# Kernel tuning notes

Measured on AMD Instinct MI355X. Metric: run time of the kernel, lower is better.

The kernel has to match this reference:

```python
import jax, jax.numpy as jnp
import numpy as np

N = 100000
F = 128

def shifted_softplus(x):
    return jax.nn.softplus(x) - jnp.log(2.0).astype(x.dtype)

def setup_inputs() -> dict:
    key = jax.random.key(0)
    ks = jax.random.split(key, 8)
    scale = 1.0 / np.sqrt(F)
    s = jax.random.normal(ks[0], (N, F), dtype=jnp.float32)
    v = jax.random.normal(ks[1], (N, F, 3), dtype=jnp.float32)
    U_w = jax.random.uniform(ks[2], (F, F), dtype=jnp.float32, minval=-scale, maxval=scale)
    V_w = jax.random.uniform(ks[3], (F, F), dtype=jnp.float32, minval=-scale, maxval=scale)
    scale2 = 1.0 / np.sqrt(2 * F)
    a_w1 = jax.random.uniform(ks[4], (F, 2 * F), dtype=jnp.float32, minval=-scale2, maxval=scale2)
    a_b1 = jax.random.uniform(ks[5], (F,), dtype=jnp.float32, minval=-scale2, maxval=scale2)
    a_w2 = jax.random.uniform(ks[6], (3 * F, F), dtype=jnp.float32, minval=-scale, maxval=scale)
    a_b2 = jax.random.uniform(ks[7], (3 * F,), dtype=jnp.float32, minval=-scale, maxval=scale)
    return {"s": s, "v": v, "U_w": U_w, "V_w": V_w,
            "a_w1": a_w1, "a_b1": a_b1, "a_w2": a_w2, "a_b2": a_b2}

def reference(s, v, U_w, V_w, a_w1, a_b1, a_w2, a_b2):
    # Vector linears along feature dim: (N,F,3) x (Fout,Fin) -> (N,F,3)
    Uv = jnp.einsum('nfc,gf->ngc', v, U_w)
    Vv = jnp.einsum('nfc,gf->ngc', v, V_w)
    Vv_norm_sq = jnp.sum(Vv * Vv, axis=-1)          # (N,F)
    mlp_in = jnp.concatenate([s, Vv_norm_sq], axis=-1)  # (N,2F)
    h = shifted_softplus(mlp_in @ a_w1.T + a_b1)     # (N,F)
    a = h @ a_w2.T + a_b2                            # (N,3F)
    a_ss, a_sv, a_vv = jnp.split(a, 3, axis=-1)
    inner = jnp.sum(Uv * Vv, axis=-1)                # (N,F)
    s_new = s + a_ss + a_sv * inner
    v_new = v + a_vv[:, :, None] * Uv
    return (s_new, v_new)
```

## Files before the change

### kernel.cpp

```cpp
#include <hip/hip_runtime.h>

#define F 128
#define TILE 32
#define NTHR 512
#define NBLK 256

typedef __attribute__((ext_vector_type(8))) __bf16 bf16x8;
typedef __attribute__((ext_vector_type(4))) float f32x4;
typedef __attribute__((ext_vector_type(8))) unsigned short us8;
typedef __attribute__((ext_vector_type(4))) unsigned short us4;
typedef __attribute__((ext_vector_type(2))) unsigned short us2;

struct f3 { float x, y, z; };

__device__ __forceinline__ unsigned short f2bf(float x) {
    __bf16 h = (__bf16)x;
    return __builtin_bit_cast(unsigned short, h);
}
__device__ __forceinline__ float bf2f(unsigned short u) {
    unsigned x = ((unsigned)u) << 16;
    return __builtin_bit_cast(float, x);
}
__device__ __forceinline__ bf16x8 pack8(float4 a, float4 b) {
    us8 t;
    t[0] = f2bf(a.x); t[1] = f2bf(a.y); t[2] = f2bf(a.z); t[3] = f2bf(a.w);
    t[4] = f2bf(b.x); t[5] = f2bf(b.y); t[6] = f2bf(b.z); t[7] = f2bf(b.w);
    return __builtin_bit_cast(bf16x8, t);
}

__device__ __forceinline__ void gload16(const float* g, const unsigned short* l) {
    __builtin_amdgcn_global_load_lds(
        (const __attribute__((address_space(1))) void*)g,
        (__attribute__((address_space(3))) void*)l, 16, 0, 0);
}

#define RAWV 0
#define A1B  24576
#define A1S  136
#define A2B  37632
#define A2S  264
#define A3B  46080
#define A3S  136
#define SHSZ 50432

__global__ __launch_bounds__(256)
void prep_w(const float* __restrict__ Uw, const float* __restrict__ Vw,
            const float* __restrict__ aw1, const float* __restrict__ aw2,
            unsigned short* __restrict__ wbf)
{
    int i = (blockIdx.x * 256 + threadIdx.x) * 4;
    const float* src; int off;
    if (i < 16384)      { src = Uw;  off = i; }
    else if (i < 32768) { src = Vw;  off = i - 16384; }
    else if (i < 65536) { src = aw1; off = i - 32768; }
    else                { src = aw2; off = i - 65536; }
    float4 x = *(const float4*)&src[off];
    us4 o;
    o[0] = f2bf(x.x); o[1] = f2bf(x.y); o[2] = f2bf(x.z); o[3] = f2bf(x.w);
    *(us4*)&wbf[i] = o;
}

template<bool PRE>
__global__ __launch_bounds__(NTHR) __attribute__((amdgpu_waves_per_eu(2, 2)))
void painn_main(const float* __restrict__ s, const float* __restrict__ v,
                const float* __restrict__ Uw, const float* __restrict__ Vw,
                const float* __restrict__ aw1, const float* __restrict__ ab1,
                const float* __restrict__ aw2, const float* __restrict__ ab2,
                const unsigned short* __restrict__ wbf,
                float* __restrict__ out, int Ntot)
{
    __shared__ __align__(16) unsigned short SH[SHSZ];

    const int tid  = threadIdx.x;
    const int lane = tid & 63;
    const int w    = tid >> 6;
    const int l15  = lane & 15;
    const int kp   = lane >> 4;
    const int col  = (w << 4) | l15;
    const size_t NF = (size_t)Ntot * F;
    const int NT   = Ntot / TILE;

    const unsigned short* wU  = wbf;
    const unsigned short* wV  = wbf + 16384;
    const unsigned short* wW1 = wbf + 32768;
    const unsigned short* wW2 = wbf + 65536;

    const float b1  = ab1[col];
    const float bss = ab2[col];
    const float bsv = ab2[F + col];
    const float bvv = ab2[2 * F + col];

    const int vf0  = lane << 1;
    const int srow = tid >> 4;
    const int sf0  = (tid & 15) << 3;

    const float* rawv = (const float*)&SH[RAWV];

    float4 sp0, sp1;

    {
        int t0 = blockIdx.x;
        const float* vsrc = v + (size_t)t0 * TILE * 384;
        #pragma unroll
        for (int j = 0; j < 6; ++j) {
            int ofs = (w + j * 8) * 256;
            gload16(vsrc + ofs + lane * 4, &SH[RAWV + ofs * 2]);
        }
        const float* ssrc = s + (size_t)t0 * TILE * 128 + srow * 128 + sf0;
        sp0 = *(const float4*)ssrc;
        sp1 = *(const float4*)(ssrc + 4);
    }
    asm volatile("s_waitcnt vmcnt(0)" ::: "memory");

    for (int t = blockIdx.x; t < NT; t += NBLK) {
        asm volatile("s_waitcnt vmcnt(8)" ::: "memory");
        __builtin_amdgcn_s_barrier();

        bf16x8 bU[4], bV[4], bW1[8], bWs[4], bWt[4], bWv[4];
        if constexpr (PRE) {
            #pragma unroll
            for (int ks = 0; ks < 4; ++ks) {
                int k0 = (ks << 5) + (kp << 3);
                bU[ks]  = *(const bf16x8*)&wU[col * F + k0];
                bV[ks]  = *(const bf16x8*)&wV[col * F + k0];
                bWs[ks] = *(const bf16x8*)&wW2[(0 * F + col) * F + k0];
                bWt[ks] = *(const bf16x8*)&wW2[(1 * F + col) * F + k0];
                bWv[ks] = *(const bf16x8*)&wW2[(2 * F + col) * F + k0];
            }
            #pragma unroll
            for (int ks = 0; ks < 8; ++ks) {
                int k0 = (ks << 5) + (kp << 3);
                bW1[ks] = *(const bf16x8*)&wW1[col * 256 + k0];
            }
        } else {
            #pragma unroll
            for (int ks = 0; ks < 4; ++ks) {
                int k0 = (ks << 5) + (kp << 3);
                const float4* p;
                p = (const float4*)&Uw[col * F + k0];              bU[ks]  = pack8(p[0], p[1]);
                p = (const float4*)&Vw[col * F + k0];              bV[ks]  = pack8(p[0], p[1]);
                p = (const float4*)&aw2[(size_t)(0*F+col)*F + k0]; bWs[ks] = pack8(p[0], p[1]);
                p = (const float4*)&aw2[(size_t)(1*F+col)*F + k0]; bWt[ks] = pack8(p[0], p[1]);
                p = (const float4*)&aw2[(size_t)(2*F+col)*F + k0]; bWv[ks] = pack8(p[0], p[1]);
            }
            #pragma unroll
            for (int ks = 0; ks < 8; ++ks) {
                int k0 = (ks << 5) + (kp << 3);
                const float4* p = (const float4*)&aw1[col * 256 + k0];
                bW1[ks] = pack8(p[0], p[1]);
            }
        }
        __builtin_amdgcn_sched_barrier(0);

        #pragma unroll
        for (int it = 0; it < 4; ++it) {
            int nl = w + (it << 3);
            const float2* src = (const float2*)&rawv[nl * 384 + vf0 * 3];
            float2 ab = src[0], cd = src[1], ef = src[2];
            us2 p;
            p[0] = f2bf(ab.x); p[1] = f2bf(cd.y); *(us2*)&SH[A1B + (0 * TILE + nl) * A1S + vf0] = p;
            p[0] = f2bf(ab.y); p[1] = f2bf(ef.x); *(us2*)&SH[A1B + (1 * TILE + nl) * A1S + vf0] = p;
            p[0] = f2bf(cd.x); p[1] = f2bf(ef.y); *(us2*)&SH[A1B + (2 * TILE + nl) * A1S + vf0] = p;
        }
        {
            us4 t0, t1;
            t0[0] = f2bf(sp0.x); t0[1] = f2bf(sp0.y); t0[2] = f2bf(sp0.z); t0[3] = f2bf(sp0.w);
            t1[0] = f2bf(sp1.x); t1[1] = f2bf(sp1.y); t1[2] = f2bf(sp1.z); t1[3] = f2bf(sp1.w);
            *(us4*)&SH[A2B + srow * A2S + sf0]     = t0;
            *(us4*)&SH[A2B + srow * A2S + sf0 + 4] = t1;
        }
        asm volatile("s_waitcnt lgkmcnt(0)" ::: "memory");
        __builtin_amdgcn_s_barrier();
        __builtin_amdgcn_sched_barrier(0);

        if (t + NBLK < NT) {
            int t2 = t + NBLK;
            const float* vsrc = v + (size_t)t2 * TILE * 384;
            #pragma unroll
            for (int j = 0; j < 6; ++j) {
                int ofs = (w + j * 8) * 256;
                gload16(vsrc + ofs + lane * 4, &SH[RAWV + ofs * 2]);
            }
            const float* ssrc = s + (size_t)t2 * TILE * 128 + srow * 128 + sf0;
            sp0 = *(const float4*)ssrc;
            sp1 = *(const float4*)(ssrc + 4);
        }
        __builtin_amdgcn_sched_barrier(0);

        float inr[2][4], nrm[2][4];
        us4 pU[6];
        #pragma unroll
        for (int nt = 0; nt < 2; ++nt)
            #pragma unroll
            for (int r = 0; r < 4; ++r) { inr[nt][r] = 0.f; nrm[nt][r] = 0.f; }
        #pragma unroll
        for (int c = 0; c < 3; ++c) {
            f32x4 aU[2], aV[2];
            aU[0] = (f32x4){0.f,0.f,0.f,0.f}; aU[1] = (f32x4){0.f,0.f,0.f,0.f};
            aV[0] = (f32x4){0.f,0.f,0.f,0.f}; aV[1] = (f32x4){0.f,0.f,0.f,0.f};
            #pragma unroll
            for (int ks = 0; ks < 4; ++ks) {
                #pragma unroll
                for (int nt = 0; nt < 2; ++nt) {
                    bf16x8 a = *(const bf16x8*)&SH[A1B + ((c * 2 + nt) * 16 + l15) * A1S + (ks << 5) + (kp << 3)];
                    aU[nt] = __builtin_amdgcn_mfma_f32_16x16x32_bf16(a, bU[ks], aU[nt], 0, 0, 0);
                    aV[nt] = __builtin_amdgcn_mfma_f32_16x16x32_bf16(a, bV[ks], aV[nt], 0, 0, 0);
                }
            }
            #pragma unroll
            for (int nt = 0; nt < 2; ++nt) {
                us4 q;
                #pragma unroll
                for (int r = 0; r < 4; ++r) {
                    nrm[nt][r] += aV[nt][r] * aV[nt][r];
                    inr[nt][r] += aU[nt][r] * aV[nt][r];
                    q[r] = f2bf(aU[nt][r]);
                }
                pU[c * 2 + nt] = q;
            }
        }
        #pragma unroll
        for (int nt = 0; nt < 2; ++nt) {
            #pragma unroll
            for (int r = 0; r < 4; ++r) {
                int row = nt * 16 + (kp << 2) + r;
                SH[A2B + row * A2S + 128 + col] = f2bf(nrm[nt][r]);
            }
        }
        asm volatile("s_waitcnt lgkmcnt(0)" ::: "memory");
        __builtin_amdgcn_s_barrier();

        f32x4 accH[2];
        accH[0] = (f32x4){0.f,0.f,0.f,0.f}; accH[1] = (f32x4){0.f,0.f,0.f,0.f};
        #pragma unroll
        for (int ks = 0; ks < 8; ++ks) {
            int k0 = (ks << 5) + (kp << 3);
            #pragma unroll
            for (int nt = 0; nt < 2; ++nt) {
                bf16x8 a = *(const bf16x8*)&SH[A2B + (nt * 16 + l15) * A2S + k0];
                accH[nt] = __builtin_amdgcn_mfma_f32_16x16x32_bf16(a, bW1[ks], accH[nt], 0, 0, 0);
            }
        }
        #pragma unroll
        for (int nt = 0; nt < 2; ++nt) {
            #pragma unroll
            for (int r = 0; r < 4; ++r) {
                float x = accH[nt][r] + b1;
                float hsp = fmaxf(x, 0.f) + __logf(1.f + __expf(-fabsf(x))) - 0.69314718056f;
                int row = nt * 16 + (kp << 2) + r;
                SH[A3B + row * A3S + col] = f2bf(hsp);
            }
        }
        asm volatile("s_waitcnt lgkmcnt(0)" ::: "memory");
        __builtin_amdgcn_s_barrier();

        f32x4 accA[2], accS[2], accT[2];
        #pragma unroll
        for (int i = 0; i < 2; ++i) {
            accA[i] = (f32x4){0.f,0.f,0.f,0.f};
            accS[i] = (f32x4){0.f,0.f,0.f,0.f};
            accT[i] = (f32x4){0.f,0.f,0.f,0.f};
        }
        #pragma unroll
        for (int ks = 0; ks < 4; ++ks) {
            int k0 = (ks << 5) + (kp << 3);
            #pragma unroll
            for (int nt = 0; nt < 2; ++nt) {
                bf16x8 a = *(const bf16x8*)&SH[A3B + (nt * 16 + l15) * A3S + k0];
                accS[nt] = __builtin_amdgcn_mfma_f32_16x16x32_bf16(a, bWs[ks], accS[nt], 0, 0, 0);
                accT[nt] = __builtin_amdgcn_mfma_f32_16x16x32_bf16(a, bWt[ks], accT[nt], 0, 0, 0);
                accA[nt] = __builtin_amdgcn_mfma_f32_16x16x32_bf16(a, bWv[ks], accA[nt], 0, 0, 0);
            }
        }

        #pragma unroll
        for (int nt = 0; nt < 2; ++nt) {
            #pragma unroll
            for (int r = 0; r < 4; ++r) {
                int nl = nt * 16 + (kp << 2) + r;
                int n  = t * TILE + nl;
                float avv = accA[nt][r] + bvv;
                size_t base = ((size_t)n * F + col) * 3;
                f3 val;
                val.x = bf2f(SH[A1B + (0 * TILE + nl) * A1S + col]) + avv * bf2f(pU[0 * 2 + nt][r]);
                val.y = bf2f(SH[A1B + (1 * TILE + nl) * A1S + col]) + avv * bf2f(pU[1 * 2 + nt][r]);
                val.z = bf2f(SH[A1B + (2 * TILE + nl) * A1S + col]) + avv * bf2f(pU[2 * 2 + nt][r]);
                *(f3*)&out[NF + base] = val;
                float sres = bf2f(SH[A2B + nl * A2S + col]);
                out[(size_t)n * F + col] = sres + (accS[nt][r] + bss) + (accT[nt][r] + bsv) * inr[nt][r];
            }
        }
    }
}

extern "C" void kernel_launch(void* const* d_in, const int* in_sizes, int n_in,
                              void* d_out, int out_size, void* d_ws, size_t ws_size,
                              hipStream_t stream) {
    (void)n_in; (void)out_size;
    const float* s   = (const float*)d_in[0];
    const float* v   = (const float*)d_in[1];
    const float* Uw  = (const float*)d_in[2];
    const float* Vw  = (const float*)d_in[3];
    const float* aw1 = (const float*)d_in[4];
    const float* ab1 = (const float*)d_in[5];
    const float* aw2 = (const float*)d_in[6];
    const float* ab2 = (const float*)d_in[7];
    float* out = (float*)d_out;
    int Ntot = in_sizes[0] / F;

    if (ws_size >= 114688u * sizeof(unsigned short)) {
        unsigned short* wbf = (unsigned short*)d_ws;
        hipLaunchKernelGGL(prep_w, dim3(112), dim3(256), 0, stream, Uw, Vw, aw1, aw2, wbf);
        hipLaunchKernelGGL((painn_main<true>), dim3(NBLK), dim3(NTHR), 0, stream,
                           s, v, Uw, Vw, aw1, ab1, aw2, ab2, wbf, out, Ntot);
    } else {
        hipLaunchKernelGGL((painn_main<false>), dim3(NBLK), dim3(NTHR), 0, stream,
                           s, v, Uw, Vw, aw1, ab1, aw2, ab2, (const unsigned short*)nullptr, out, Ntot);
    }
}
```

Measured before the change: 187.2 us.

## Replace persistent pipelined kernel with one-tile-per-block non-persistent grid

Drops the persistent 256-block loop with software prefetch of the next tile. Instead it launches one 256-thread block per 16-row tile (6250 blocks), and each wave now computes two 16-column groups. Weights are reloaded from global/L2 per block for the W1/W2 stages rather than kept in registers across tiles, and LDS use is halved so more blocks can be resident per CU. The aim is to rely on occupancy and hardware scheduling to hide latency, at the cost of repeated weight loads and losing the explicit load/compute overlap.

Result: slower. 212.7 us (+13.6%).

```diff
diff --git a/kernel.cpp b/kernel.cpp
--- a/kernel.cpp
+++ b/kernel.cpp
@@ -1,9 +1,8 @@
 #include <hip/hip_runtime.h>
 
 #define F 128
-#define TILE 32
-#define NTHR 512
-#define NBLK 256
+#define TILE 16
+#define NTHR 256
 
 typedef __attribute__((ext_vector_type(8))) __bf16 bf16x8;
 typedef __attribute__((ext_vector_type(4))) float f32x4;
@@ -35,13 +34,13 @@
 }
 
 #define RAWV 0
-#define A1B  24576
+#define A1B  12288
 #define A1S  136
-#define A2B  37632
+#define A2B  18816
 #define A2S  264
-#define A3B  46080
+#define A3B  23040
 #define A3S  136
-#define SHSZ 50432
+#define SHSZ 25216
 
 __global__ __launch_bounds__(256)
 void prep_w(const float* __restrict__ Uw, const float* __restrict__ Vw,
@@ -61,7 +60,7 @@
 }
 
 template<bool PRE>
-__global__ __launch_bounds__(NTHR) __attribute__((amdgpu_waves_per_eu(2, 2)))
+__global__ __launch_bounds__(NTHR) __attribute__((amdgpu_waves_per_eu(3)))
 void painn_main(const float* __restrict__ s, const float* __restrict__ v,
                 const float* __restrict__ Uw, const float* __restrict__ Vw,
                 const float* __restrict__ aw1, const float* __restrict__ ab1,
@@ -76,20 +75,16 @@
     const int w    = tid >> 6;
     const int l15  = lane & 15;
     const int kp   = lane >> 4;
-    const int col  = (w << 4) | l15;
+    const int colA = (w << 4) | l15;
+    const int colB = 64 + ((w << 4) | l15);
     const size_t NF = (size_t)Ntot * F;
-    const int NT   = Ntot / TILE;
+    const int t    = blockIdx.x;
 
     const unsigned short* wU  = wbf;
     const unsigned short* wV  = wbf + 16384;
     const unsigned short* wW1 = wbf + 32768;
     const unsigned short* wW2 = wbf + 65536;
 
-    const float b1  = ab1[col];
-    const float bss = ab2[col];
-    const float bsv = ab2[F + col];
-    const float bvv = ab2[2 * F + col];
-
     const int vf0  = lane << 1;
     const int srow = tid >> 4;
     const int sf0  = (tid & 15) << 3;
@@ -97,198 +92,187 @@
     const float* rawv = (const float*)&SH[RAWV];
 
     float4 sp0, sp1;
-
     {
-        int t0 = blockIdx.x;
-        const float* vsrc = v + (size_t)t0 * TILE * 384;
-        #pragma unroll
-        for (int j = 0; j < 6; ++j) {
-            int ofs = (w + j * 8) * 256;
-            gload16(vsrc + ofs + lane * 4, &SH[RAWV + ofs * 2]);
-        }
-        const float* ssrc = s + (size_t)t0 * TILE * 128 + srow * 128 + sf0;
+        const float* ssrc = s + (size_t)t * TILE * 128 + srow * 128 + sf0;
         sp0 = *(const float4*)ssrc;
         sp1 = *(const float4*)(ssrc + 4);
     }
+    bf16x8 bU[2][4], bV[2][4];
+    #pragma unroll
+    for (int g = 0; g < 2; ++g) {
+        int colg = g ? colB : colA;
+        #pragma unroll
+        for (int ks = 0; ks < 4; ++ks) {
+            int k0 = (ks << 5) + (kp << 3);
+            if constexpr (PRE) {
+                bU[g][ks] = *(const bf16x8*)&wU[colg * F + k0];
+                bV[g][ks] = *(const bf16x8*)&wV[colg * F + k0];
+            } else {
+                const float4* pu = (const float4*)&Uw[colg * F + k0];
+                bU[g][ks] = pack8(pu[0], pu[1]);
+                const float4* pv = (const float4*)&Vw[colg * F + k0];
+                bV[g][ks] = pack8(pv[0], pv[1]);
+            }
+        }
+    }
+    {
+        const float* vsrc = v + (size_t)t * TILE * 384;
+        #pragma unroll
+        for (int j = 0; j < 6; ++j) {
+            int ofs = (w + j * 4) * 256;
+            gload16(vsrc + ofs + lane * 4, &SH[RAWV + ofs * 2]);
+        }
+    }
     asm volatile("s_waitcnt vmcnt(0)" ::: "memory");
-
-    for (int t = blockIdx.x; t < NT; t += NBLK) {
-        asm volatile("s_waitcnt vmcnt(8)" ::: "memory");
-        __builtin_amdgcn_s_barrier();
-
-        bf16x8 bU[4], bV[4], bW1[8], bWs[4], bWt[4], bWv[4];
-        if constexpr (PRE) {
+    __builtin_amdgcn_s_barrier();
+
+    #pragma unroll
+    for (int it = 0; it < 4; ++it) {
+        int idx = tid + it * 256;
+        int nl  = idx >> 6;
+        int f0  = (idx & 63) << 1;
+        const float2* src = (const float2*)&rawv[nl * 384 + f0 * 3];
+        float2 ab = src[0], cd = src[1], ef = src[2];
+        us2 p;
+        p[0] = f2bf(ab.x); p[1] = f2bf(cd.y); *(us2*)&SH[A1B + (0 * TILE + nl) * A1S + f0] = p;
+        p[0] = f2bf(ab.y); p[1] = f2bf(ef.x); *(us2*)&SH[A1B + (1 * TILE + nl) * A1S + f0] = p;
+        p[0] = f2bf(cd.x); p[1] = f2bf(ef.y); *(us2*)&SH[A1B + (2 * TILE + nl) * A1S + f0] = p;
+    }
+    {
+        us4 t0, t1;
+        t0[0] = f2bf(sp0.x); t0[1] = f2bf(sp0.y); t0[2] = f2bf(sp0.z); t0[3] = f2bf(sp0.w);
+        t1[0] = f2bf(sp1.x); t1[1] = f2bf(sp1.y); t1[2] = f2bf(sp1.z); t1[3] = f2bf(sp1.w);
+        *(us4*)&SH[A2B + srow * A2S + sf0]     = t0;
+        *(us4*)&SH[A2B + srow * A2S + sf0 + 4] = t1;
+    }
+    asm volatile("s_waitcnt lgkmcnt(0)" ::: "memory");
+    __builtin_amdgcn_s_barrier();
+
+    float nrm[2][4], inr[2][4];
+    us4 pU[2][3];
+    #pragma unroll
+    for (int c = 0; c < 3; ++c) {
+        f32x4 aU[2], aV[2];
+        aU[0] = (f32x4){0.f,0.f,0.f,0.f}; aU[1] = (f32x4){0.f,0.f,0.f,0.f};
+        aV[0] = (f32x4){0.f,0.f,0.f,0.f}; aV[1] = (f32x4){0.f,0.f,0.f,0.f};
+        #pragma unroll
+        for (int ks = 0; ks < 4; ++ks) {
+            bf16x8 a = *(const bf16x8*)&SH[A1B + (c * TILE + l15) * A1S + (ks << 5) + (kp << 3)];
             #pragma unroll
-            for (int ks = 0; ks < 4; ++ks) {
-                int k0 = (ks << 5) + (kp << 3);
-                bU[ks]  = *(const bf16x8*)&wU[col * F + k0];
-                bV[ks]  = *(const bf16x8*)&wV[col * F + k0];
-                bWs[ks] = *(const bf16x8*)&wW2[(0 * F + col) * F + k0];
-                bWt[ks] = *(const bf16x8*)&wW2[(1 * F + col) * F + k0];
-                bWv[ks] = *(const bf16x8*)&wW2[(2 * F + col) * F + k0];
-            }
-            #pragma unroll
-            for (int ks = 0; ks < 8; ++ks) {
-                int k0 = (ks << 5) + (kp << 3);
-                bW1[ks] = *(const bf16x8*)&wW1[col * 256 + k0];
-            }
-        } else {
-            #pragma unroll
-            for (int ks = 0; ks < 4; ++ks) {
-                int k0 = (ks << 5) + (kp << 3);
-                const float4* p;
-                p = (const float4*)&Uw[col * F + k0];              bU[ks]  = pack8(p[0], p[1]);
-                p = (const float4*)&Vw[col * F + k0];              bV[ks]  = pack8(p[0], p[1]);
-                p = (const float4*)&aw2[(size_t)(0*F+col)*F + k0]; bWs[ks] = pack8(p[0], p[1]);
-                p = (const float4*)&aw2[(size_t)(1*F+col)*F + k0]; bWt[ks] = pack8(p[0], p[1]);
-                p = (const float4*)&aw2[(size_t)(2*F+col)*F + k0]; bWv[ks] = pack8(p[0], p[1]);
-            }
-            #pragma unroll
-            for (int ks = 0; ks < 8; ++ks) {
-                int k0 = (ks << 5) + (kp << 3);
-                const float4* p = (const float4*)&aw1[col * 256 + k0];
-                bW1[ks] = pack8(p[0], p[1]);
-            }
-        }
-        __builtin_amdgcn_sched_barrier(0);
-
-        #pragma unroll
-        for (int it = 0; it < 4; ++it) {
-            int nl = w + (it << 3);
-            const float2* src = (const float2*)&rawv[nl * 384 + vf0 * 3];
-            float2 ab = src[0], cd = src[1], ef = src[2];
-            us2 p;
-            p[0] = f2bf(ab.x); p[1] = f2bf(cd.y); *(us2*)&SH[A1B + (0 * TILE + nl) * A1S + vf0] = p;
-            p[0] = f2bf(ab.y); p[1] = f2bf(ef.x); *(us2*)&SH[A1B + (1 * TILE + nl) * A1S + vf0] = p;
-            p[0] = f2bf(cd.x); p[1] = f2bf(ef.y); *(us2*)&SH[A1B + (2 * TILE + nl) * A1S + vf0] = p;
-        }
-        {
-            us4 t0, t1;
-            t0[0] = f2bf(sp0.x); t0[1] = f2bf(sp0.y); t0[2] = f2bf(sp0.z); t0[3] = f2bf(sp0.w);
-            t1[0] = f2bf(sp1.x); t1[1] = f2bf(sp1.y); t1[2] = f2bf(sp1.z); t1[3] = f2bf(sp1.w);
-            *(us4*)&SH[A2B + srow * A2S + sf0]     = t0;
-            *(us4*)&SH[A2B + srow * A2S + sf0 + 4] = t1;
-        }
-        asm volatile("s_waitcnt lgkmcnt(0)" ::: "memory");
-        __builtin_amdgcn_s_barrier();
-        __builtin_amdgcn_sched_barrier(0);
-
-        if (t + NBLK < NT) {
-            int t2 = t + NBLK;
-            const float* vsrc = v + (size_t)t2 * TILE * 384;
-            #pragma unroll
-            for (int j = 0; j < 6; ++j) {
-                int ofs = (w + j * 8) * 256;
-                gload16(vsrc + ofs + lane * 4, &SH[RAWV + ofs * 2]);
-            }
-            const float* ssrc = s + (size_t)t2 * TILE * 128 + srow * 128 + sf0;
-            sp0 = *(const float4*)ssrc;
-            sp1 = *(const float4*)(ssrc + 4);
-        }
-        __builtin_amdgcn_sched_barrier(0);
-
-        float inr[2][4], nrm[2][4];
-        us4 pU[6];
-        #pragma unroll
-        for (int nt = 0; nt < 2; ++nt)
-            #pragma unroll
-            for (int r = 0; r < 4; ++r) { inr[nt][r] = 0.f; nrm[nt][r] = 0.f; }
-        #pragma unroll
-        for (int c = 0; c < 3; ++c) {
-            f32x4 aU[2], aV[2];
-            aU[0] = (f32x4){0.f,0.f,0.f,0.f}; aU[1] = (f32x4){0.f,0.f,0.f,0.f};
-            aV[0] = (f32x4){0.f,0.f,0.f,0.f}; aV[1] = (f32x4){0.f,0.f,0.f,0.f};
-            #pragma unroll
-            for (int ks = 0; ks < 4; ++ks) {
-                #pragma unroll
-                for (int nt = 0; nt < 2; ++nt) {
-                    bf16x8 a = *(const bf16x8*)&SH[A1B + ((c * 2 + nt) * 16 + l15) * A1S + (ks << 5) + (kp << 3)];
-                    aU[nt] = __builtin_amdgcn_mfma_f32_16x16x32_bf16(a, bU[ks], aU[nt], 0, 0, 0);
-                    aV[nt] = __builtin_amdgcn_mfma_f32_16x16x32_bf16(a, bV[ks], aV[nt], 0, 0, 0);
-                }
-            }
-            #pragma unroll
-            for (int nt = 0; nt < 2; ++nt) {
-                us4 q;
-                #pragma unroll
-                for (int r = 0; r < 4; ++r) {
-                    nrm[nt][r] += aV[nt][r] * aV[nt][r];
-                    inr[nt][r] += aU[nt][r] * aV[nt][r];
-                    q[r] = f2bf(aU[nt][r]);
-                }
-                pU[c * 2 + nt] = q;
-            }
-        }
-        #pragma unroll
-        for (int nt = 0; nt < 2; ++nt) {
+            for (int g = 0; g < 2; ++g) {
+                aU[g] = __builtin_amdgcn_mfma_f32_16x16x32_bf16(a, bU[g][ks], aU[g], 0, 0, 0);
+                aV[g] = __builtin_amdgcn_mfma_f32_16x16x32_bf16(a, bV[g][ks], aV[g], 0, 0, 0);
+            }
+        }
+        #pragma unroll
+        for (int g = 0; g < 2; ++g) {
+            us4 q;
             #pragma unroll
             for (int r = 0; r < 4; ++r) {
-                int row = nt * 16 + (kp << 2) + r;
-                SH[A2B + row * A2S + 128 + col] = f2bf(nrm[nt][r]);
-            }
-        }
-        asm volatile("s_waitcnt lgkmcnt(0)" ::: "memory");
-        __builtin_amdgcn_s_barrier();
-
-        f32x4 accH[2];
-        accH[0] = (f32x4){0.f,0.f,0.f,0.f}; accH[1] = (f32x4){0.f,0.f,0.f,0.f};
-        #pragma unroll
-        for (int ks = 0; ks < 8; ++ks) {
-            int k0 = (ks << 5) + (kp << 3);
-            #pragma unroll
-            for (int nt = 0; nt < 2; ++nt) {
-                bf16x8 a = *(const bf16x8*)&SH[A2B + (nt * 16 + l15) * A2S + k0];
-                accH[nt] = __builtin_amdgcn_mfma_f32_16x16x32_bf16(a, bW1[ks], accH[nt], 0, 0, 0);
-            }
-        }
-        #pragma unroll
-        for (int nt = 0; nt < 2; ++nt) {
-            #pragma unroll
-            for (int r = 0; r < 4; ++r) {
-                float x = accH[nt][r] + b1;
-                float hsp = fmaxf(x, 0.f) + __logf(1.f + __expf(-fabsf(x))) - 0.69314718056f;
-                int row = nt * 16 + (kp << 2) + r;
-                SH[A3B + row * A3S + col] = f2bf(hsp);
-            }
-        }
-        asm volatile("s_waitcnt lgkmcnt(0)" ::: "memory");
-        __builtin_amdgcn_s_barrier();
-
-        f32x4 accA[2], accS[2], accT[2];
-        #pragma unroll
-        for (int i = 0; i < 2; ++i) {
-            accA[i] = (f32x4){0.f,0.f,0.f,0.f};
-            accS[i] = (f32x4){0.f,0.f,0.f,0.f};
-            accT[i] = (f32x4){0.f,0.f,0.f,0.f};
-        }
-        #pragma unroll
-        for (int ks = 0; ks < 4; ++ks) {
-            int k0 = (ks << 5) + (kp << 3);
-            #pragma unroll
-            for (int nt = 0; nt < 2; ++nt) {
-                bf16x8 a = *(const bf16x8*)&SH[A3B + (nt * 16 + l15) * A3S + k0];
-                accS[nt] = __builtin_amdgcn_mfma_f32_16x16x32_bf16(a, bWs[ks], accS[nt], 0, 0, 0);
-                accT[nt] = __builtin_amdgcn_mfma_f32_16x16x32_bf16(a, bWt[ks], accT[nt], 0, 0, 0);
-                accA[nt] = __builtin_amdgcn_mfma_f32_16x16x32_bf16(a, bWv[ks], accA[nt], 0, 0, 0);
-            }
-        }
-
-        #pragma unroll
-        for (int nt = 0; nt < 2; ++nt) {
-            #pragma unroll
-            for (int r = 0; r < 4; ++r) {
-                int nl = nt * 16 + (kp << 2) + r;
-                int n  = t * TILE + nl;
-                float avv = accA[nt][r] + bvv;
-                size_t base = ((size_t)n * F + col) * 3;
-                f3 val;
-                val.x = bf2f(SH[A1B + (0 * TILE + nl) * A1S + col]) + avv * bf2f(pU[0 * 2 + nt][r]);
-                val.y = bf2f(SH[A1B + (1 * TILE + nl) * A1S + col]) + avv * bf2f(pU[1 * 2 + nt][r]);
-                val.z = bf2f(SH[A1B + (2 * TILE + nl) * A1S + col]) + avv * bf2f(pU[2 * 2 + nt][r]);
-                *(f3*)&out[NF + base] = val;
-                float sres = bf2f(SH[A2B + nl * A2S + col]);
-                out[(size_t)n * F + col] = sres + (accS[nt][r] + bss) + (accT[nt][r] + bsv) * inr[nt][r];
-            }
+                float uu = aU[g][r], vv = aV[g][r];
+                if (c == 0) { nrm[g][r] = vv * vv; inr[g][r] = uu * vv; }
+                else        { nrm[g][r] += vv * vv; inr[g][r] += uu * vv; }
+                q[r] = f2bf(uu);
+            }
+            pU[g][c] = q;
+        }
+    }
+    #pragma unroll
+    for (int r = 0; r < 4; ++r) {
+        int row = (kp << 2) + r;
+        SH[A2B + row * A2S + 128 + colA] = f2bf(nrm[0][r]);
+        SH[A2B + row * A2S + 128 + colB] = f2bf(nrm[1][r]);
+    }
+    asm volatile("s_waitcnt lgkmcnt(0)" ::: "memory");
+    __builtin_amdgcn_s_barrier();
+
+    f32x4 accH[2];
+    accH[0] = (f32x4){0.f,0.f,0.f,0.f}; accH[1] = (f32x4){0.f,0.f,0.f,0.f};
+    #pragma unroll
+    for (int ks = 0; ks < 8; ++ks) {
+        int k0 = (ks << 5) + (kp << 3);
+        bf16x8 a = *(const bf16x8*)&SH[A2B + l15 * A2S + k0];
+        #pragma unroll
+        for (int g = 0; g < 2; ++g) {
+            int colg = g ? colB : colA;
+            bf16x8 bw;
+            if constexpr (PRE) {
+                bw = *(const bf16x8*)&wW1[colg * 256 + k0];
+            } else {
+                const float4* p = (const float4*)&aw1[colg * 256 + k0];
+                bw = pack8(p[0], p[1]);
+            }
+            accH[g] = __builtin_amdgcn_mfma_f32_16x16x32_bf16(a, bw, accH[g], 0, 0, 0);
+        }
+    }
+    {
+        float b1A = ab1[colA], b1B = ab1[colB];
+        #pragma unroll
+        for (int r = 0; r < 4; ++r) {
+            int row = (kp << 2) + r;
+            float xA = accH[0][r] + b1A;
+            float xB = accH[1][r] + b1B;
+            float hA = fmaxf(xA, 0.f) + __logf(1.f + __expf(-fabsf(xA))) - 0.69314718056f;
+            float hB = fmaxf(xB, 0.f) + __logf(1.f + __expf(-fabsf(xB))) - 0.69314718056f;
+            SH[A3B + row * A3S + colA] = f2bf(hA);
+            SH[A3B + row * A3S + colB] = f2bf(hB);
+        }
+    }
+    asm volatile("s_waitcnt lgkmcnt(0)" ::: "memory");
+    __builtin_amdgcn_s_barrier();
+
+    f32x4 accS[2], accT[2], accA[2];
+    #pragma unroll
+    for (int i = 0; i < 2; ++i) {
+        accS[i] = (f32x4){0.f,0.f,0.f,0.f};
+        accT[i] = (f32x4){0.f,0.f,0.f,0.f};
+        accA[i] = (f32x4){0.f,0.f,0.f,0.f};
+    }
+    #pragma unroll
+    for (int ks = 0; ks < 4; ++ks) {
+        int k0 = (ks << 5) + (kp << 3);
+        bf16x8 a = *(const bf16x8*)&SH[A3B + l15 * A3S + k0];
+        #pragma unroll
+        for (int g = 0; g < 2; ++g) {
+            int colg = g ? colB : colA;
+            bf16x8 bws, bwt, bwv;
+            if constexpr (PRE) {
+                bws = *(const bf16x8*)&wW2[(0 * F + colg) * F + k0];
+                bwt = *(const bf16x8*)&wW2[(1 * F + colg) * F + k0];
+                bwv = *(const bf16x8*)&wW2[(2 * F + colg) * F + k0];
+            } else {
+                const float4* p0 = (const float4*)&aw2[(size_t)(0 * F + colg) * F + k0];
+                const float4* p1 = (const float4*)&aw2[(size_t)(1 * F + colg) * F + k0];
+                const float4* p2 = (const float4*)&aw2[(size_t)(2 * F + colg) * F + k0];
+                bws = pack8(p0[0], p0[1]);
+                bwt = pack8(p1[0], p1[1]);
+                bwv = pack8(p2[0], p2[1]);
+            }
+            accS[g] = __builtin_amdgcn_mfma_f32_16x16x32_bf16(a, bws, accS[g], 0, 0, 0);
+            accT[g] = __builtin_amdgcn_mfma_f32_16x16x32_bf16(a, bwt, accT[g], 0, 0, 0);
+            accA[g] = __builtin_amdgcn_mfma_f32_16x16x32_bf16(a, bwv, accA[g], 0, 0, 0);
+        }
+    }
+
+    #pragma unroll
+    for (int g = 0; g < 2; ++g) {
+        int colg = g ? colB : colA;
+        float bss = ab2[colg];
+        float bsv = ab2[F + colg];
+        float bvv = ab2[2 * F + colg];
+        #pragma unroll
+        for (int r = 0; r < 4; ++r) {
+            int nl = (kp << 2) + r;
+            int n  = t * TILE + nl;
+            float avv = accA[g][r] + bvv;
+            size_t base = ((size_t)n * F + colg) * 3;
+            f3 val;
+            val.x = bf2f(SH[A1B + (0 * TILE + nl) * A1S + colg]) + avv * bf2f(pU[g][0][r]);
+            val.y = bf2f(SH[A1B + (1 * TILE + nl) * A1S + colg]) + avv * bf2f(pU[g][1][r]);
+            val.z = bf2f(SH[A1B + (2 * TILE + nl) * A1S + colg]) + avv * bf2f(pU[g][2][r]);
+            *(f3*)&out[NF + base] = val;
+            float sres = bf2f(SH[A2B + nl * A2S + colg]);
+            out[(size_t)n * F + colg] = sres + (accS[g][r] + bss) + (accT[g][r] + bsv) * inr[g][r];
         }
     }
 }
@@ -307,14 +291,15 @@
     const float* ab2 = (const float*)d_in[7];
     float* out = (float*)d_out;
     int Ntot = in_sizes[0] / F;
+    int NT   = Ntot / TILE;
 
     if (ws_size >= 114688u * sizeof(unsigned short)) {
         unsigned short* wbf = (unsigned short*)d_ws;
         hipLaunchKernelGGL(prep_w, dim3(112), dim3(256), 0, stream, Uw, Vw, aw1, aw2, wbf);
-        hipLaunchKernelGGL((painn_main<true>), dim3(NBLK), dim3(NTHR), 0, stream,
+        hipLaunchKernelGGL((painn_main<true>), dim3(NT), dim3(NTHR), 0, stream,
                            s, v, Uw, Vw, aw1, ab1, aw2, ab2, wbf, out, Ntot);
     } else {
-        hipLaunchKernelGGL((painn_main<false>), dim3(NBLK), dim3(NTHR), 0, stream,
+        hipLaunchKernelGGL((painn_main<false>), dim3(NT), dim3(NTHR), 0, stream,
                            s, v, Uw, Vw, aw1, ab1, aw2, ab2, (const unsigned short*)nullptr, out, Ntot);
     }
 }
```

## Enlarge node tile to 48 rows with swizzled LDS layout and bounds handling

Applied to the files above, without the earlier changes.

Raises the per-block node tile from 32 to 48, so each loaded weight fragment feeds three MFMA row-tiles instead of two, and the prefetch grows to 9 async v loads per tile. The padded v-row LDS layout becomes an XOR-swizzled unpadded layout, tail tiles are handled by clamped loads and guarded stores, and the W2 fragment loads move later to ease register pressure. LDS use rises to about 149 KB with more registers live, and with 2 waves per EU this may limit occupancy or cause spills. The tile count of 2084 is no longer a multiple of the 256 blocks, so the work is less evenly balanced.

After: 413.6 us. 121% more time.

```diff
diff --git a/kernel.cpp b/kernel.cpp
--- a/kernel.cpp
+++ b/kernel.cpp
@@ -1,7 +1,7 @@
 #include <hip/hip_runtime.h>
 
 #define F 128
-#define TILE 32
+#define TILE 48
 #define NTHR 512
 #define NBLK 256
 
@@ -35,13 +35,16 @@
 }
 
 #define RAWV 0
-#define A1B  24576
-#define A1S  136
-#define A2B  37632
+#define VRB  36864
+#define A2B  55296
 #define A2S  264
-#define A3B  46080
+#define A3B  67968
 #define A3S  136
-#define SHSZ 50432
+#define SHSZ 74496
+
+__device__ __forceinline__ int vr_idx(int crow, int k) {
+    return VRB + (((crow << 7) + k) ^ ((crow & 7) << 3));
+}
 
 __global__ __launch_bounds__(256)
 void prep_w(const float* __restrict__ Uw, const float* __restrict__ Vw,
@@ -78,7 +81,8 @@
     const int kp   = lane >> 4;
     const int col  = (w << 4) | l15;
     const size_t NF = (size_t)Ntot * F;
-    const int NT   = Ntot / TILE;
+    const int NT   = (Ntot + TILE - 1) / TILE;
+    const size_t vmax = (size_t)Ntot * 384 - 256;
 
     const unsigned short* wU  = wbf;
     const unsigned short* wV  = wbf + 16384;
@@ -90,159 +94,175 @@
     const float bsv = ab2[F + col];
     const float bvv = ab2[2 * F + col];
 
-    const int vf0  = lane << 1;
-    const int srow = tid >> 4;
-    const int sf0  = (tid & 15) << 3;
-
     const float* rawv = (const float*)&SH[RAWV];
-
-    float4 sp0, sp1;
+    float4 sreg[3];
 
     {
         int t0 = blockIdx.x;
-        const float* vsrc = v + (size_t)t0 * TILE * 384;
-        #pragma unroll
-        for (int j = 0; j < 6; ++j) {
-            int ofs = (w + j * 8) * 256;
-            gload16(vsrc + ofs + lane * 4, &SH[RAWV + ofs * 2]);
-        }
-        const float* ssrc = s + (size_t)t0 * TILE * 128 + srow * 128 + sf0;
-        sp0 = *(const float4*)ssrc;
-        sp1 = *(const float4*)(ssrc + 4);
+        #pragma unroll
+        for (int j = 0; j < 9; ++j) {
+            size_t ofs = (size_t)t0 * 18432 + (w + j * 8) * 256;
+            if (ofs > vmax) ofs = vmax;
+            gload16(v + ofs + lane * 4, &SH[RAWV + (size_t)(w + j * 8) * 512]);
+        }
+        #pragma unroll
+        for (int it = 0; it < 3; ++it) {
+            int idx = tid + it * 512;
+            int row = idx >> 5;
+            int f0  = (idx & 31) << 2;
+            int gr  = t0 * TILE + row; if (gr >= Ntot) gr = Ntot - 1;
+            sreg[it] = *(const float4*)&s[(size_t)gr * 128 + f0];
+        }
     }
     asm volatile("s_waitcnt vmcnt(0)" ::: "memory");
 
     for (int t = blockIdx.x; t < NT; t += NBLK) {
-        asm volatile("s_waitcnt vmcnt(8)" ::: "memory");
+        asm volatile("s_waitcnt vmcnt(16)" ::: "memory");
         __builtin_amdgcn_s_barrier();
 
-        bf16x8 bU[4], bV[4], bW1[8], bWs[4], bWt[4], bWv[4];
-        if constexpr (PRE) {
+        bf16x8 bU[4], bV[4], bW1[8];
+        #pragma unroll
+        for (int ks = 0; ks < 4; ++ks) {
+            int k0 = (ks << 5) + (kp << 3);
+            if constexpr (PRE) {
+                bU[ks] = *(const bf16x8*)&wU[col * F + k0];
+                bV[ks] = *(const bf16x8*)&wV[col * F + k0];
+            } else {
+                const float4* pu = (const float4*)&Uw[col * F + k0];
+                bU[ks] = pack8(pu[0], pu[1]);
+                const float4* pv = (const float4*)&Vw[col * F + k0];
+                bV[ks] = pack8(pv[0], pv[1]);
+            }
+        }
+        #pragma unroll
+        for (int ks = 0; ks < 8; ++ks) {
+            int k0 = (ks << 5) + (kp << 3);
+            if constexpr (PRE) {
+                bW1[ks] = *(const bf16x8*)&wW1[col * 256 + k0];
+            } else {
+                const float4* p = (const float4*)&aw1[col * 256 + k0];
+                bW1[ks] = pack8(p[0], p[1]);
+            }
+        }
+        __builtin_amdgcn_sched_barrier(0);
+
+        #pragma unroll
+        for (int it = 0; it < 6; ++it) {
+            int idx = tid + it * 512;
+            int nl  = idx >> 6;
+            int f0  = (idx & 63) << 1;
+            const float2* src = (const float2*)&rawv[nl * 384 + f0 * 3];
+            float2 ab = src[0], cd = src[1], ef = src[2];
+            us2 p;
+            p[0] = f2bf(ab.x); p[1] = f2bf(cd.y); *(us2*)&SH[vr_idx(0 * TILE + nl, f0)] = p;
+            p[0] = f2bf(ab.y); p[1] = f2bf(ef.x); *(us2*)&SH[vr_idx(1 * TILE + nl, f0)] = p;
+            p[0] = f2bf(cd.x); p[1] = f2bf(ef.y); *(us2*)&SH[vr_idx(2 * TILE + nl, f0)] = p;
+        }
+        #pragma unroll
+        for (int it = 0; it < 3; ++it) {
+            int idx = tid + it * 512;
+            int row = idx >> 5;
+            int f0  = (idx & 31) << 2;
+            us4 t0;
+            t0[0] = f2bf(sreg[it].x); t0[1] = f2bf(sreg[it].y);
+            t0[2] = f2bf(sreg[it].z); t0[3] = f2bf(sreg[it].w);
+            *(us4*)&SH[A2B + row * A2S + f0] = t0;
+        }
+        asm volatile("s_waitcnt lgkmcnt(0)" ::: "memory");
+        __builtin_amdgcn_s_barrier();
+
+        if (t + NBLK < NT) {
+            int t2 = t + NBLK;
+            #pragma unroll
+            for (int j = 0; j < 9; ++j) {
+                size_t ofs = (size_t)t2 * 18432 + (w + j * 8) * 256;
+                if (ofs > vmax) ofs = vmax;
+                gload16(v + ofs + lane * 4, &SH[RAWV + (size_t)(w + j * 8) * 512]);
+            }
+            #pragma unroll
+            for (int it = 0; it < 3; ++it) {
+                int idx = tid + it * 512;
+                int row = idx >> 5;
+                int f0  = (idx & 31) << 2;
+                int gr  = t2 * TILE + row; if (gr >= Ntot) gr = Ntot - 1;
+                sreg[it] = *(const float4*)&s[(size_t)gr * 128 + f0];
+            }
+        }
+        __builtin_amdgcn_sched_barrier(0);
+
+        float nrm[3][4], inr[3][4];
+        us4 pU[9];
+        #pragma unroll
+        for (int c = 0; c < 3; ++c) {
+            f32x4 aU[3], aV[3];
+            #pragma unroll
+            for (int nt = 0; nt < 3; ++nt) { aU[nt] = (f32x4){0.f,0.f,0.f,0.f}; aV[nt] = (f32x4){0.f,0.f,0.f,0.f}; }
             #pragma unroll
             for (int ks = 0; ks < 4; ++ks) {
-                int k0 = (ks << 5) + (kp << 3);
-                bU[ks]  = *(const bf16x8*)&wU[col * F + k0];
-                bV[ks]  = *(const bf16x8*)&wV[col * F + k0];
+                #pragma unroll
+                for (int nt = 0; nt < 3; ++nt) {
+                    int crow = c * TILE + nt * 16 + l15;
+                    bf16x8 a = *(const bf16x8*)&SH[vr_idx(crow, (ks << 5) + (kp << 3))];
+                    aU[nt] = __builtin_amdgcn_mfma_f32_16x16x32_bf16(a, bU[ks], aU[nt], 0, 0, 0);
+                    aV[nt] = __builtin_amdgcn_mfma_f32_16x16x32_bf16(a, bV[ks], aV[nt], 0, 0, 0);
+                }
+            }
+            #pragma unroll
+            for (int nt = 0; nt < 3; ++nt) {
+                us4 q;
+                #pragma unroll
+                for (int r = 0; r < 4; ++r) {
+                    float uu = aU[nt][r], vv = aV[nt][r];
+                    if (c == 0) { nrm[nt][r] = vv * vv; inr[nt][r] = uu * vv; }
+                    else        { nrm[nt][r] += vv * vv; inr[nt][r] += uu * vv; }
+                    q[r] = f2bf(uu);
+                }
+                pU[c * 3 + nt] = q;
+            }
+        }
+        #pragma unroll
+        for (int nt = 0; nt < 3; ++nt) {
+            #pragma unroll
+            for (int r = 0; r < 4; ++r) {
+                int row = nt * 16 + (kp << 2) + r;
+                SH[A2B + row * A2S + 128 + col] = f2bf(nrm[nt][r]);
+            }
+        }
+
+        bf16x8 bWs[4], bWt[4], bWv[4];
+        #pragma unroll
+        for (int ks = 0; ks < 4; ++ks) {
+            int k0 = (ks << 5) + (kp << 3);
+            if constexpr (PRE) {
                 bWs[ks] = *(const bf16x8*)&wW2[(0 * F + col) * F + k0];
                 bWt[ks] = *(const bf16x8*)&wW2[(1 * F + col) * F + k0];
                 bWv[ks] = *(const bf16x8*)&wW2[(2 * F + col) * F + k0];
-            }
-            #pragma unroll
-            for (int ks = 0; ks < 8; ++ks) {
-                int k0 = (ks << 5) + (kp << 3);
-                bW1[ks] = *(const bf16x8*)&wW1[col * 256 + k0];
-            }
-        } else {
-            #pragma unroll
-            for (int ks = 0; ks < 4; ++ks) {
-                int k0 = (ks << 5) + (kp << 3);
-                const float4* p;
-                p = (const float4*)&Uw[col * F + k0];              bU[ks]  = pack8(p[0], p[1]);
-                p = (const float4*)&Vw[col * F + k0];              bV[ks]  = pack8(p[0], p[1]);
-                p = (const float4*)&aw2[(size_t)(0*F+col)*F + k0]; bWs[ks] = pack8(p[0], p[1]);
-                p = (const float4*)&aw2[(size_t)(1*F+col)*F + k0]; bWt[ks] = pack8(p[0], p[1]);
-                p = (const float4*)&aw2[(size_t)(2*F+col)*F + k0]; bWv[ks] = pack8(p[0], p[1]);
-            }
-            #pragma unroll
-            for (int ks = 0; ks < 8; ++ks) {
-                int k0 = (ks << 5) + (kp << 3);
-                const float4* p = (const float4*)&aw1[col * 256 + k0];
-                bW1[ks] = pack8(p[0], p[1]);
-            }
-        }
-        __builtin_amdgcn_sched_barrier(0);
-
-        #pragma unroll
-        for (int it = 0; it < 4; ++it) {
-            int nl = w + (it << 3);
-            const float2* src = (const float2*)&rawv[nl * 384 + vf0 * 3];
-            float2 ab = src[0], cd = src[1], ef = src[2];
-            us2 p;
-            p[0] = f2bf(ab.x); p[1] = f2bf(cd.y); *(us2*)&SH[A1B + (0 * TILE + nl) * A1S + vf0] = p;
-            p[0] = f2bf(ab.y); p[1] = f2bf(ef.x); *(us2*)&SH[A1B + (1 * TILE + nl) * A1S + vf0] = p;
-            p[0] = f2bf(cd.x); p[1] = f2bf(ef.y); *(us2*)&SH[A1B + (2 * TILE + nl) * A1S + vf0] = p;
-        }
-        {
-            us4 t0, t1;
-            t0[0] = f2bf(sp0.x); t0[1] = f2bf(sp0.y); t0[2] = f2bf(sp0.z); t0[3] = f2bf(sp0.w);
-            t1[0] = f2bf(sp1.x); t1[1] = f2bf(sp1.y); t1[2] = f2bf(sp1.z); t1[3] = f2bf(sp1.w);
-            *(us4*)&SH[A2B + srow * A2S + sf0]     = t0;
-            *(us4*)&SH[A2B + srow * A2S + sf0 + 4] = t1;
+            } else {
+                const float4* p0 = (const float4*)&aw2[(size_t)(0 * F + col) * F + k0];
+                const float4* p1 = (const float4*)&aw2[(size_t)(1 * F + col) * F + k0];
+                const float4* p2 = (const float4*)&aw2[(size_t)(2 * F + col) * F + k0];
+                bWs[ks] = pack8(p0[0], p0[1]);
+                bWt[ks] = pack8(p1[0], p1[1]);
+                bWv[ks] = pack8(p2[0], p2[1]);
+            }
         }
         asm volatile("s_waitcnt lgkmcnt(0)" ::: "memory");
         __builtin_amdgcn_s_barrier();
-        __builtin_amdgcn_sched_barrier(0);
-
-        if (t + NBLK < NT) {
-            int t2 = t + NBLK;
-            const float* vsrc = v + (size_t)t2 * TILE * 384;
-            #pragma unroll
-            for (int j = 0; j < 6; ++j) {
-                int ofs = (w + j * 8) * 256;
-                gload16(vsrc + ofs + lane * 4, &SH[RAWV + ofs * 2]);
-            }
-            const float* ssrc = s + (size_t)t2 * TILE * 128 + srow * 128 + sf0;
-            sp0 = *(const float4*)ssrc;
-            sp1 = *(const float4*)(ssrc + 4);
-        }
-        __builtin_amdgcn_sched_barrier(0);
-
-        float inr[2][4], nrm[2][4];
-        us4 pU[6];
-        #pragma unroll
-        for (int nt = 0; nt < 2; ++nt)
-            #pragma unroll
-            for (int r = 0; r < 4; ++r) { inr[nt][r] = 0.f; nrm[nt][r] = 0.f; }
-        #pragma unroll
-        for (int c = 0; c < 3; ++c) {
-            f32x4 aU[2], aV[2];
-            aU[0] = (f32x4){0.f,0.f,0.f,0.f}; aU[1] = (f32x4){0.f,0.f,0.f,0.f};
-            aV[0] = (f32x4){0.f,0.f,0.f,0.f}; aV[1] = (f32x4){0.f,0.f,0.f,0.f};
-            #pragma unroll
-            for (int ks = 0; ks < 4; ++ks) {
-                #pragma unroll
-                for (int nt = 0; nt < 2; ++nt) {
-                    bf16x8 a = *(const bf16x8*)&SH[A1B + ((c * 2 + nt) * 16 + l15) * A1S + (ks << 5) + (kp << 3)];
-                    aU[nt] = __builtin_amdgcn_mfma_f32_16x16x32_bf16(a, bU[ks], aU[nt], 0, 0, 0);
-                    aV[nt] = __builtin_amdgcn_mfma_f32_16x16x32_bf16(a, bV[ks], aV[nt], 0, 0, 0);
-                }
-            }
-            #pragma unroll
-            for (int nt = 0; nt < 2; ++nt) {
-                us4 q;
-                #pragma unroll
-                for (int r = 0; r < 4; ++r) {
-                    nrm[nt][r] += aV[nt][r] * aV[nt][r];
-                    inr[nt][r] += aU[nt][r] * aV[nt][r];
-                    q[r] = f2bf(aU[nt][r]);
-                }
-                pU[c * 2 + nt] = q;
-            }
-        }
-        #pragma unroll
-        for (int nt = 0; nt < 2; ++nt) {
-            #pragma unroll
-            for (int r = 0; r < 4; ++r) {
-                int row = nt * 16 + (kp << 2) + r;
-                SH[A2B + row * A2S + 128 + col] = f2bf(nrm[nt][r]);
-            }
-        }
-        asm volatile("s_waitcnt lgkmcnt(0)" ::: "memory");
-        __builtin_amdgcn_s_barrier();
-
-        f32x4 accH[2];
-        accH[0] = (f32x4){0.f,0.f,0.f,0.f}; accH[1] = (f32x4){0.f,0.f,0.f,0.f};
+
+        f32x4 accH[3];
+        #pragma unroll
+        for (int nt = 0; nt < 3; ++nt) accH[nt] = (f32x4){0.f,0.f,0.f,0.f};
         #pragma unroll
         for (int ks = 0; ks < 8; ++ks) {
             int k0 = (ks << 5) + (kp << 3);
             #pragma unroll
-            for (int nt = 0; nt < 2; ++nt) {
+            for (int nt = 0; nt < 3; ++nt) {
                 bf16x8 a = *(const bf16x8*)&SH[A2B + (nt * 16 + l15) * A2S + k0];
                 accH[nt] = __builtin_amdgcn_mfma_f32_16x16x32_bf16(a, bW1[ks], accH[nt], 0, 0, 0);
             }
         }
         #pragma unroll
-        for (int nt = 0; nt < 2; ++nt) {
+        for (int nt = 0; nt < 3; ++nt) {
             #pragma unroll
             for (int r = 0; r < 4; ++r) {
                 float x = accH[nt][r] + b1;
@@ -254,18 +274,18 @@
         asm volatile("s_waitcnt lgkmcnt(0)" ::: "memory");
         __builtin_amdgcn_s_barrier();
 
-        f32x4 accA[2], accS[2], accT[2];
-        #pragma unroll
-        for (int i = 0; i < 2; ++i) {
-            accA[i] = (f32x4){0.f,0.f,0.f,0.f};
+        f32x4 accS[3], accT[3], accA[3];
+        #pragma unroll
+        for (int i = 0; i < 3; ++i) {
             accS[i] = (f32x4){0.f,0.f,0.f,0.f};
             accT[i] = (f32x4){0.f,0.f,0.f,0.f};
+            accA[i] = (f32x4){0.f,0.f,0.f,0.f};
         }
         #pragma unroll
         for (int ks = 0; ks < 4; ++ks) {
             int k0 = (ks << 5) + (kp << 3);
             #pragma unroll
-            for (int nt = 0; nt < 2; ++nt) {
+            for (int nt = 0; nt < 3; ++nt) {
                 bf16x8 a = *(const bf16x8*)&SH[A3B + (nt * 16 + l15) * A3S + k0];
                 accS[nt] = __builtin_amdgcn_mfma_f32_16x16x32_bf16(a, bWs[ks], accS[nt], 0, 0, 0);
                 accT[nt] = __builtin_amdgcn_mfma_f32_16x16x32_bf16(a, bWt[ks], accT[nt], 0, 0, 0);
@@ -274,20 +294,22 @@
         }
 
         #pragma unroll
-        for (int nt = 0; nt < 2; ++nt) {
+        for (int nt = 0; nt < 3; ++nt) {
             #pragma unroll
             for (int r = 0; r < 4; ++r) {
                 int nl = nt * 16 + (kp << 2) + r;
                 int n  = t * TILE + nl;
-                float avv = accA[nt][r] + bvv;
-                size_t base = ((size_t)n * F + col) * 3;
-                f3 val;
-                val.x = bf2f(SH[A1B + (0 * TILE + nl) * A1S + col]) + avv * bf2f(pU[0 * 2 + nt][r]);
-                val.y = bf2f(SH[A1B + (1 * TILE + nl) * A1S + col]) + avv * bf2f(pU[1 * 2 + nt][r]);
-                val.z = bf2f(SH[A1B + (2 * TILE + nl) * A1S + col]) + avv * bf2f(pU[2 * 2 + nt][r]);
-                *(f3*)&out[NF + base] = val;
-                float sres = bf2f(SH[A2B + nl * A2S + col]);
-                out[(size_t)n * F + col] = sres + (accS[nt][r] + bss) + (accT[nt][r] + bsv) * inr[nt][r];
+                if (n < Ntot) {
+                    float avv = accA[nt][r] + bvv;
+                    size_t base = ((size_t)n * F + col) * 3;
+                    f3 val;
+                    val.x = bf2f(SH[vr_idx(0 * TILE + nl, col)]) + avv * bf2f(pU[0 * 3 + nt][r]);
+                    val.y = bf2f(SH[vr_idx(1 * TILE + nl, col)]) + avv * bf2f(pU[1 * 3 + nt][r]);
+                    val.z = bf2f(SH[vr_idx(2 * TILE + nl, col)]) + avv * bf2f(pU[2 * 3 + nt][r]);
+                    *(f3*)&out[NF + base] = val;
+                    float sres = bf2f(SH[A2B + nl * A2S + col]);
+                    out[(size_t)n * F + col] = sres + (accS[nt][r] + bss) + (accT[nt][r] + bsv) * inr[nt][r];
+                }
             }
         }
     }
```
